# Optimization experiments

Hardware: AMD Instinct MI355X
Metric: run time of the kernel (lower is better)

## Reference

```python
import jax, jax.numpy as jnp
import numpy as np

B, S, HID, NH = 4, 4096, 1024, 16
D = HID // NH
EPS = 1e-5


def setup_inputs() -> dict:
    key = jax.random.key(0)
    ks = jax.random.split(key, 8)
    x = jax.random.normal(ks[0], (B, S, HID), dtype=jnp.float32)
    sc = 0.03  # ~xavier for 1024x1024
    Wq = jax.random.normal(ks[1], (HID, HID), dtype=jnp.float32) * sc
    Wk = jax.random.normal(ks[2], (HID, HID), dtype=jnp.float32) * sc
    Wv = jax.random.normal(ks[3], (HID, HID), dtype=jnp.float32) * sc
    Wbeta = jax.random.normal(ks[4], (HID, NH), dtype=jnp.float32) * sc
    b_beta = jnp.full((NH,), 0.9, dtype=jnp.float32)  # init.constant_(0.9)
    Wo = jax.random.normal(ks[5], (HID, HID), dtype=jnp.float32) * sc
    b_o = jnp.zeros((HID,), dtype=jnp.float32)
    ln_g = jnp.ones((HID,), dtype=jnp.float32)
    ln_b = jnp.zeros((HID,), dtype=jnp.float32)
    return {"x": x, "Wq": Wq, "Wk": Wk, "Wv": Wv, "Wbeta": Wbeta,
            "b_beta": b_beta, "Wo": Wo, "b_o": b_o, "ln_g": ln_g, "ln_b": ln_b}


def _delta_scan(q, k, v, beta):
    # q,k,v: (B,S,NH,D); beta: (B,S,NH)
    # Faithful to torch einsum 'bik,bji->bjk' with broadcast over i:
    # update[b,h,:,k'] = k_t[b,h,k'] * sum_d v_t[b,h,d]  (same row repeated)
    vsum = v.sum(-1)  # (B,S,NH)
    qs = jnp.moveaxis(q, 1, 0)       # (S,B,NH,D)
    ks_ = jnp.moveaxis(k, 1, 0)
    vs = jnp.moveaxis(vsum, 1, 0)    # (S,B,NH)
    bs = jnp.moveaxis(beta, 1, 0)    # (S,B,NH)

    def step(h, inp):
        q_t, k_t, vsum_t, beta_t = inp
        h = h * beta_t[..., None, None]
        h = h + (k_t * vsum_t[..., None])[:, :, None, :]  # broadcast over rows
        o_t = jnp.einsum('bhj,bhjk->bhk', q_t, h)
        return h, o_t

    h0 = jnp.zeros((q.shape[0], q.shape[2], D, D), dtype=q.dtype)
    _, o = jax.lax.scan(step, h0, (qs, ks_, vs, bs))
    return jnp.moveaxis(o, 0, 1)  # (B,S,NH,D)


def reference(x, Wq, Wk, Wv, Wbeta, b_beta, Wo, b_o, ln_g, ln_b):
    b, s, hid = x.shape
    residual = x
    q = (x @ Wq).reshape(b, s, NH, D)
    k = (x @ Wk).reshape(b, s, NH, D)
    v = (x @ Wv).reshape(b, s, NH, D)
    beta = jax.nn.sigmoid(x @ Wbeta + b_beta)  # (B,S,NH)
    o = _delta_scan(q, k, v, beta).reshape(b, s, hid)
    out = o @ Wo + b_o  # dropout is identity in eval
    y = residual + out
    mu = y.mean(-1, keepdims=True)
    var = ((y - mu) ** 2).mean(-1, keepdims=True)
    return ln_g * (y - mu) * jax.lax.rsqrt(var + EPS) + ln_b
```

## Files before the change

### kernel.cpp

```cpp
#include <hip/hip_runtime.h>
#include <hip/hip_bf16.h>

typedef unsigned short u16;
typedef unsigned int   u32;
typedef u32 __attribute__((address_space(1))) gas_u32;
typedef u32 __attribute__((address_space(3))) las_u32;
typedef __bf16 bf16x8 __attribute__((ext_vector_type(8)));
typedef float  f32x4  __attribute__((ext_vector_type(4)));

constexpr int BATCH = 4, SEQ = 4096, HID = 1024, NH = 16, DH = 64;
constexpr int M  = BATCH * SEQ;
constexpr int KD = HID;

__device__ __forceinline__ u16 f2bf(float f) {
  __hip_bfloat16 h = __float2bfloat16(f);
  u16 u; __builtin_memcpy(&u, &h, 2); return u;
}
__device__ __forceinline__ float bf2f(u16 u) {
  u32 x = ((u32)u) << 16; float f; __builtin_memcpy(&f, &x, 4); return f;
}


__global__ __launch_bounds__(256) void transpose_cast(const float* __restrict__ Wk,
                                                      const float* __restrict__ Wo,
                                                      u16* __restrict__ WkT,
                                                      u16* __restrict__ WoT) {
  __shared__ float tile[32][33];
  const float* src = blockIdx.z ? Wo : Wk;
  u16* dst = blockIdx.z ? WoT : WkT;
  int bx = blockIdx.x * 32, by = blockIdx.y * 32;
  int tx = threadIdx.x & 31, ty = threadIdx.x >> 5;
#pragma unroll
  for (int i = 0; i < 4; i++)
    tile[ty + i * 8][tx] = src[(size_t)(by + ty + i * 8) * HID + bx + tx];
  __syncthreads();
#pragma unroll
  for (int i = 0; i < 4; i++)
    dst[(size_t)(bx + ty + i * 8) * HID + by + tx] = f2bf(tile[tx][ty + i * 8]);
}

__global__ __launch_bounds__(256) void build_wsum(const float* __restrict__ Wq,
                                                  const float* __restrict__ Wv,
                                                  const float* __restrict__ Wbeta,
                                                  u16* __restrict__ WsT) {
  int tid = blockIdx.x * 256 + threadIdx.x;
  int c = tid >> 10, kk = tid & 1023;
  float s = 0.f;
  if (c < 16)      { for (int d = 0; d < DH; d++) s += Wq[(size_t)kk * HID + c * DH + d]; }
  else if (c < 32) { for (int d = 0; d < DH; d++) s += Wv[(size_t)kk * HID + (c - 16) * DH + d]; }
  else if (c < 48) { s = Wbeta[(size_t)kk * NH + (c - 32)]; }
  WsT[(size_t)c * HID + kk] = f2bf(s);
}

__global__ __launch_bounds__(256) void skinny_fused(
    const float* __restrict__ x, const u16* __restrict__ Bt,
    const float* __restrict__ bias, float* __restrict__ sq,
    float* __restrict__ sv, float* __restrict__ sb, u16* __restrict__ xb) {
  constexpr int BM = 64, BK = 64;
  __shared__ u16 As[BM * BK];
  __shared__ u16 Bs[64 * BK];
  const int tid = threadIdx.x, wave = tid >> 6, lane = tid & 63;
  const int bm = blockIdx.x;
  const int r16 = lane & 15, hi = lane >> 4;
  const int rsub = lane >> 3, csub = (lane & 7) * 8;
  f32x4 acc[4] = {};
  const float* Ab = x + (size_t)bm * BM * KD;
  u16* xbb = xb + (size_t)bm * BM * KD;

  for (int kt = 0; kt < KD; kt += BK) {
#pragma unroll
    for (int i = 0; i < 2; i++) {
      int slot = wave * 2 + i;
      const u16* g = Bt + (size_t)(slot * 8 + rsub) * KD + kt + csub;
      __builtin_amdgcn_global_load_lds((const gas_u32*)g, (las_u32*)(Bs + slot * 512), 16, 0, 0);
    }
#pragma unroll
    for (int p = 0; p < 2; p++) {
      const int row = p * 32 + (tid >> 3);
      const int c8 = (tid & 7) * 8;
      const float4 u0 = *(const float4*)(Ab + (size_t)row * KD + kt + c8);
      const float4 u1 = *(const float4*)(Ab + (size_t)row * KD + kt + c8 + 4);
      uint4 w;
      w.x = (u32)f2bf(u0.x) | ((u32)f2bf(u0.y) << 16);
      w.y = (u32)f2bf(u0.z) | ((u32)f2bf(u0.w) << 16);
      w.z = (u32)f2bf(u1.x) | ((u32)f2bf(u1.y) << 16);
      w.w = (u32)f2bf(u1.z) | ((u32)f2bf(u1.w) << 16);
      *(uint4*)(As + row * BK + c8) = w;
      *(uint4*)(xbb + (size_t)row * KD + kt + c8) = w;
    }
    __syncthreads();
#pragma unroll
    for (int kk = 0; kk < 2; kk++) {
      bf16x8 af = *(const bf16x8*)(As + (wave * 16 + r16) * BK + kk * 32 + hi * 8);
#pragma unroll
      for (int fn = 0; fn < 4; fn++) {
        bf16x8 bfr = *(const bf16x8*)(Bs + (fn * 16 + r16) * BK + kk * 32 + hi * 8);
        acc[fn] = __builtin_amdgcn_mfma_f32_16x16x32_bf16(af, bfr, acc[fn], 0, 0, 0);
      }
    }
    __syncthreads();
  }

#pragma unroll
  for (int fn = 0; fn < 4; fn++) {
    const int col = fn * 16 + r16;
#pragma unroll
    for (int j = 0; j < 4; j++) {
      const int row = bm * BM + wave * 16 + hi * 4 + j;
      const int b = row >> 12, t = row & 4095;
      float v = acc[fn][j];
      if (col < 16)      sq[((size_t)(b * 16 + col)) * SEQ + t] = v;
      else if (col < 32) sv[((size_t)(b * 16 + col - 16)) * SEQ + t] = v;
      else if (col < 48) {
        float z = v + bias[col - 32];
        sb[((size_t)(b * 16 + col - 32)) * SEQ + t] = 1.f / (1.f + __expf(-z));
      }
    }
  }
}


__device__ __forceinline__ void stage_quarter(const u16* __restrict__ Gk,
                                              int q, u16* lds_tile, int tid, int wave) {
  const int row = q * 64 + (tid >> 3);
  const int s = tid & 7;
  const u16* g = Gk + (size_t)row * KD + (size_t)((s ^ (row & 7)) << 3);
  u16* l = lds_tile + q * 4096 + wave * 512;
  __builtin_amdgcn_global_load_lds((const gas_u32*)g, (las_u32*)l, 16, 0, 0);
}

__device__ __forceinline__ const bf16x8* lds_frag(const u16* lds_tile, int row, int cg) {
  return (const bf16x8*)(lds_tile + ((size_t)row << 6) + (size_t)((cg ^ (row & 7)) << 3));
}

template <int EPI>
__global__ __launch_bounds__(512) void gemm256(
    const u16* __restrict__ A, const u16* __restrict__ Bt, int N,
    u16* __restrict__ Cb, const u16* __restrict__ xres, const float* __restrict__ bias) {
  constexpr int BK = 64, NT = KD / BK;
  __shared__ u16 lds[2][2][16384];
  const int tid = threadIdx.x, wave = tid >> 6, lane = tid & 63;
  const int wm = wave >> 2, wn = wave & 3;
  const int r16 = lane & 15, hi = lane >> 4;
  const int nbn = N >> 8;
  const int bm = (int)blockIdx.x / nbn, bn = (int)blockIdx.x % nbn;
  const u16* Abase = A + (size_t)bm * 256 * KD;
  const u16* Bbase = Bt + (size_t)bn * 256 * KD;

  f32x4 acc[8][4] = {};

  {
    u16* la = &lds[0][0][0]; u16* lb = &lds[0][1][0];
    stage_quarter(Abase, 0, la, tid, wave);
    stage_quarter(Abase, 2, la, tid, wave);
    stage_quarter(Bbase, 0, lb, tid, wave);
    stage_quarter(Bbase, 1, lb, tid, wave);
    stage_quarter(Bbase, 2, lb, tid, wave);
    stage_quarter(Bbase, 3, lb, tid, wave);
    stage_quarter(Abase, 1, la, tid, wave);
    stage_quarter(Abase, 3, la, tid, wave);
  }
  asm volatile("s_waitcnt vmcnt(2)" ::: "memory");
  __builtin_amdgcn_s_barrier();

  for (int kt = 0; kt < NT - 1; ++kt) {
    const int cur = kt & 1;
    const u16* la = &lds[cur][0][0];
    const u16* lb = &lds[cur][1][0];
    u16* na = &lds[cur ^ 1][0][0];
    u16* nb = &lds[cur ^ 1][1][0];
    const u16* An = Abase + (kt + 1) * BK;
    const u16* Bn = Bbase + (kt + 1) * BK;

    bf16x8 bF[4][2];
#pragma unroll
    for (int ph = 0; ph < 4; ++ph) {
      const int mh = ph >> 1;
      const int kk = ph & 1;
      if (ph == 0)      { stage_quarter(An, 0, na, tid, wave); stage_quarter(An, 2, na, tid, wave); }
      else if (ph == 1) { stage_quarter(Bn, 0, nb, tid, wave); stage_quarter(Bn, 1, nb, tid, wave); }
      else if (ph == 2) { stage_quarter(Bn, 2, nb, tid, wave); stage_quarter(Bn, 3, nb, tid, wave); }
      else              { stage_quarter(An, 1, na, tid, wave); stage_quarter(An, 3, na, tid, wave); }
      bf16x8 aF[4];
#pragma unroll
      for (int f = 0; f < 4; ++f)
        aF[f] = *lds_frag(la, wm * 128 + mh * 64 + f * 16 + r16, kk * 4 + hi);
      if (ph < 2) {
#pragma unroll
        for (int g = 0; g < 4; ++g)
          bF[g][kk] = *lds_frag(lb, wn * 64 + g * 16 + r16, kk * 4 + hi);
      }
      __builtin_amdgcn_s_barrier();
      asm volatile("s_waitcnt lgkmcnt(0)" ::: "memory");
      __builtin_amdgcn_sched_barrier(0);
      __builtin_amdgcn_s_setprio(1);
#pragma unroll
      for (int f = 0; f < 4; ++f)
#pragma unroll
        for (int g = 0; g < 4; ++g)
          acc[mh * 4 + f][g] = __builtin_amdgcn_mfma_f32_16x16x32_bf16(
              aF[f], bF[g][kk], acc[mh * 4 + f][g], 0, 0, 0);
      __builtin_amdgcn_s_setprio(0);
      if (ph == 1) { asm volatile("s_waitcnt vmcnt(4)" ::: "memory"); }
      if (ph == 3) { asm volatile("s_waitcnt vmcnt(2)" ::: "memory"); }
      __builtin_amdgcn_s_barrier();
    }
  }

  {
    const u16* la = &lds[(NT - 1) & 1][0][0];
    const u16* lb = &lds[(NT - 1) & 1][1][0];
    bf16x8 bF[4][2];
#pragma unroll
    for (int ph = 0; ph < 4; ++ph) {
      const int mh = ph >> 1, kk = ph & 1;
      bf16x8 aF[4];
#pragma unroll
      for (int f = 0; f < 4; ++f)
        aF[f] = *lds_frag(la, wm * 128 + mh * 64 + f * 16 + r16, kk * 4 + hi);
      if (ph < 2) {
#pragma unroll
        for (int g = 0; g < 4; ++g)
          bF[g][kk] = *lds_frag(lb, wn * 64 + g * 16 + r16, kk * 4 + hi);
      }
      __builtin_amdgcn_s_barrier();
      asm volatile("s_waitcnt lgkmcnt(0)" ::: "memory");
      __builtin_amdgcn_sched_barrier(0);
      __builtin_amdgcn_s_setprio(1);
#pragma unroll
      for (int f = 0; f < 4; ++f)
#pragma unroll
        for (int g = 0; g < 4; ++g)
          acc[mh * 4 + f][g] = __builtin_amdgcn_mfma_f32_16x16x32_bf16(
              aF[f], bF[g][kk], acc[mh * 4 + f][g], 0, 0, 0);
      __builtin_amdgcn_s_setprio(0);
      if (ph == 1) { asm volatile("s_waitcnt vmcnt(0)" ::: "memory"); }
      __builtin_amdgcn_s_barrier();
    }
  }

#pragma unroll
  for (int fm = 0; fm < 8; ++fm) {
#pragma unroll
    for (int fn = 0; fn < 4; ++fn) {
      const int col = bn * 256 + wn * 64 + fn * 16 + r16;
#pragma unroll
      for (int j = 0; j < 4; ++j) {
        const int row = bm * 256 + wm * 128 + fm * 16 + hi * 4 + j;
        float v = acc[fm][fn][j];
        if constexpr (EPI == 2) v += bf2f(xres[(size_t)row * N + col]) + bias[col];
        Cb[(size_t)row * N + col] = f2bf(v);
      }
    }
  }
}


__global__ __launch_bounds__(256) void scan_chunks(const u16* __restrict__ kbuf,
                                                   const float* __restrict__ sv_t,
                                                   const float* __restrict__ sb_t,
                                                   float* __restrict__ Pbuf,
                                                   float* __restrict__ Rloc) {
  const int wave = threadIdx.x >> 6, lane = threadIdx.x & 63;
  const int gid = blockIdx.x * 4 + wave;
  const int seq = gid >> 6, chunk = gid & 63;
  const int b = seq >> 4, h = seq & 15;
  const int t0 = chunk * 64;
  const float bet = sb_t[(size_t)seq * SEQ + t0 + lane];
  const float vs  = sv_t[(size_t)seq * SEQ + t0 + lane];
  const u16* kp = kbuf + ((size_t)(b * SEQ + t0)) * HID + h * DH + lane;
  float r = 0.f, P = 1.f;
#pragma unroll
  for (int tt = 0; tt < 64; tt += 8) {
    u16 kr[8];
#pragma unroll
    for (int j = 0; j < 8; j++) kr[j] = kp[(size_t)(tt + j) * HID];
#pragma unroll
    for (int j = 0; j < 8; j++) {
      float bt = __shfl(bet, tt + j);
      float vt = __shfl(vs, tt + j);
      r = fmaf(r, bt, bf2f(kr[j]) * vt);
      P *= bt;
    }
  }
  Rloc[(size_t)gid * 64 + lane] = r;
  if (lane == 0) Pbuf[gid] = P;
}

__global__ __launch_bounds__(64) void scan_prefix(const float* __restrict__ Pbuf,
                                                  const float* __restrict__ Rloc,
                                                  float* __restrict__ Rin) {
  const int seq = blockIdx.x, lane = threadIdx.x;
  const float* pp = Pbuf + seq * 64;
  const float* rl = Rloc + (size_t)seq * 64 * 64 + lane;
  float* ri = Rin + (size_t)seq * 64 * 64 + lane;
  float rin = 0.f;
#pragma unroll
  for (int c0 = 0; c0 < 64; c0 += 8) {
    float P[8], L[8];
#pragma unroll
    for (int j = 0; j < 8; j++) { P[j] = pp[c0 + j]; L[j] = rl[(size_t)(c0 + j) * 64]; }
#pragma unroll
    for (int j = 0; j < 8; j++) {
      ri[(size_t)(c0 + j) * 64] = rin;
      rin = fmaf(P[j], rin, L[j]);
    }
  }
}

__global__ __launch_bounds__(256) void scan_apply(const u16* __restrict__ kbuf,
                                                  const float* __restrict__ sq_t,
                                                  const float* __restrict__ sv_t,
                                                  const float* __restrict__ sb_t,
                                                  const float* __restrict__ Rin,
                                                  u16* __restrict__ obuf) {
  const int wave = threadIdx.x >> 6, lane = threadIdx.x & 63;
  const int gid = blockIdx.x * 4 + wave;
  const int seq = gid >> 6, chunk = gid & 63;
  const int b = seq >> 4, h = seq & 15;
  const int t0 = chunk * 64;
  const float bet = sb_t[(size_t)seq * SEQ + t0 + lane];
  const float vs  = sv_t[(size_t)seq * SEQ + t0 + lane];
  const float qs  = sq_t[(size_t)seq * SEQ + t0 + lane];
  const u16* kp = kbuf + ((size_t)(b * SEQ + t0)) * HID + h * DH + lane;
  u16* op = obuf + ((size_t)(b * SEQ + t0)) * HID + h * DH + lane;
  float r = Rin[(size_t)gid * 64 + lane];
#pragma unroll
  for (int tt = 0; tt < 64; tt += 8) {
    u16 kr[8];
#pragma unroll
    for (int j = 0; j < 8; j++) kr[j] = kp[(size_t)(tt + j) * HID];
#pragma unroll
    for (int j = 0; j < 8; j++) {
      float bt = __shfl(bet, tt + j);
      float vt = __shfl(vs, tt + j);
      float qt = __shfl(qs, tt + j);
      r = fmaf(r, bt, bf2f(kr[j]) * vt);
      op[(size_t)(tt + j) * HID] = f2bf(qt * r);
    }
  }
}

__global__ __launch_bounds__(256) void ln_kernel(const u16* __restrict__ y,
                                                 const float* __restrict__ g,
                                                 const float* __restrict__ bt,
                                                 float* __restrict__ out) {
  const int row = blockIdx.x;
  const u16* yr = y + (size_t)row * HID;
  const int t = threadIdx.x;
  ushort4 u = *(const ushort4*)(yr + t * 4);
  float v0 = bf2f(u.x), v1 = bf2f(u.y), v2 = bf2f(u.z), v3 = bf2f(u.w);
  float s  = v0 + v1 + v2 + v3;
  float ss = v0 * v0 + v1 * v1 + v2 * v2 + v3 * v3;
#pragma unroll
  for (int m = 1; m < 64; m <<= 1) { s += __shfl_xor(s, m); ss += __shfl_xor(ss, m); }
  __shared__ float red[8];
  const int wave = t >> 6, lane = t & 63;
  if (lane == 0) { red[wave] = s; red[4 + wave] = ss; }
  __syncthreads();
  float st  = red[0] + red[1] + red[2] + red[3];
  float sst = red[4] + red[5] + red[6] + red[7];
  float mu  = st * (1.f / 1024.f);
  float var = sst * (1.f / 1024.f) - mu * mu;
  float inv = rsqrtf(var + 1e-5f);
  const int c = t * 4;
  float4 o;
  o.x = g[c + 0] * ((v0 - mu) * inv) + bt[c + 0];
  o.y = g[c + 1] * ((v1 - mu) * inv) + bt[c + 1];
  o.z = g[c + 2] * ((v2 - mu) * inv) + bt[c + 2];
  o.w = g[c + 3] * ((v3 - mu) * inv) + bt[c + 3];
  *(float4*)(out + (size_t)row * HID + c) = o;
}

extern "C" void kernel_launch(void* const* d_in, const int* in_sizes, int n_in,
                              void* d_out, int out_size, void* d_ws, size_t ws_size,
                              hipStream_t stream) {
  const float* x     = (const float*)d_in[0];
  const float* Wq    = (const float*)d_in[1];
  const float* Wk    = (const float*)d_in[2];
  const float* Wv    = (const float*)d_in[3];
  const float* Wbeta = (const float*)d_in[4];
  const float* bbeta = (const float*)d_in[5];
  const float* Wo    = (const float*)d_in[6];
  const float* b_o   = (const float*)d_in[7];
  const float* ln_g  = (const float*)d_in[8];
  const float* ln_b  = (const float*)d_in[9];
  float* out = (float*)d_out;

  char* ws = (char*)d_ws;
  size_t off = 0;
  auto alloc = [&](size_t bytes) {
    char* p = ws + off; off += (bytes + 255) & ~(size_t)255; return p;
  };
  u16* xb   = (u16*)alloc((size_t)M * HID * 2);
  u16* kbuf = (u16*)alloc((size_t)M * HID * 2);
  u16* obuf = (u16*)alloc((size_t)M * HID * 2);
  u16* WkT  = (u16*)alloc((size_t)HID * HID * 2);
  u16* WoT  = (u16*)alloc((size_t)HID * HID * 2);
  u16* WsT  = (u16*)alloc((size_t)64 * HID * 2);
  float* sq_t = (float*)alloc((size_t)64 * SEQ * 4);
  float* sv_t = (float*)alloc((size_t)64 * SEQ * 4);
  float* sb_t = (float*)alloc((size_t)64 * SEQ * 4);
  float* Pbuf = (float*)alloc((size_t)4096 * 4);
  float* Rloc = (float*)alloc((size_t)4096 * 64 * 4);
  float* Rin  = (float*)alloc((size_t)4096 * 64 * 4);
  u16* ybuf = kbuf;

  transpose_cast<<<dim3(32, 32, 2), 256, 0, stream>>>(Wk, Wo, WkT, WoT);
  build_wsum<<<256, 256, 0, stream>>>(Wq, Wv, Wbeta, WsT);

  skinny_fused<<<M / 64, 256, 0, stream>>>(x, WsT, bbeta, sq_t, sv_t, sb_t, xb);

  gemm256<0><<<(M / 256) * (HID / 256), 512, 0, stream>>>(
      xb, WkT, HID, kbuf, nullptr, nullptr);

  scan_chunks<<<1024, 256, 0, stream>>>(kbuf, sv_t, sb_t, Pbuf, Rloc);
  scan_prefix<<<64, 64, 0, stream>>>(Pbuf, Rloc, Rin);
  scan_apply<<<1024, 256, 0, stream>>>(kbuf, sq_t, sv_t, sb_t, Rin, obuf);

  gemm256<2><<<(M / 256) * (HID / 256), 512, 0, stream>>>(
      obuf, WoT, HID, ybuf, xb, b_o);

  ln_kernel<<<M, 256, 0, stream>>>(ybuf, ln_g, ln_b, out);
}
```

Measured before the change: 158.4 us.

## Merge GEMM main loop phases from four to two per K-tile

Restructures the GEMM inner K-loop from four phases with a barrier each into two half-tile phases. Each phase loads both kk fragments from LDS and issues 32 MFMAs. The explicit lgkmcnt waits and sched_barriers are dropped, so the compiler can interleave LDS reads with MFMAs. This halves the barriers per K-tile and gives longer MFMA runs, at the cost of more live fragment registers, which may hurt occupancy or cause spills.

```diff
diff --git a/kernel.cpp b/kernel.cpp
--- a/kernel.cpp
+++ b/kernel.cpp
@@ -172,71 +172,98 @@
     const u16* An = Abase + (kt + 1) * BK;
     const u16* Bn = Bbase + (kt + 1) * BK;
 
-    bf16x8 bF[4][2];
-#pragma unroll
-    for (int ph = 0; ph < 4; ++ph) {
-      const int mh = ph >> 1;
-      const int kk = ph & 1;
-      if (ph == 0)      { stage_quarter(An, 0, na, tid, wave); stage_quarter(An, 2, na, tid, wave); }
-      else if (ph == 1) { stage_quarter(Bn, 0, nb, tid, wave); stage_quarter(Bn, 1, nb, tid, wave); }
-      else if (ph == 2) { stage_quarter(Bn, 2, nb, tid, wave); stage_quarter(Bn, 3, nb, tid, wave); }
-      else              { stage_quarter(An, 1, na, tid, wave); stage_quarter(An, 3, na, tid, wave); }
-      bf16x8 aF[4];
-#pragma unroll
-      for (int f = 0; f < 4; ++f)
-        aF[f] = *lds_frag(la, wm * 128 + mh * 64 + f * 16 + r16, kk * 4 + hi);
-      if (ph < 2) {
+    stage_quarter(An, 0, na, tid, wave);
+    stage_quarter(An, 2, na, tid, wave);
+    bf16x8 bF[4][2], aF0[4][2];
+#pragma unroll
+    for (int kk = 0; kk < 2; ++kk) {
+#pragma unroll
+      for (int f = 0; f < 4; ++f)
+        aF0[f][kk] = *lds_frag(la, wm * 128 + f * 16 + r16, kk * 4 + hi);
+#pragma unroll
+      for (int g = 0; g < 4; ++g)
+        bF[g][kk] = *lds_frag(lb, wn * 64 + g * 16 + r16, kk * 4 + hi);
+    }
+    stage_quarter(Bn, 0, nb, tid, wave);
+    stage_quarter(Bn, 1, nb, tid, wave);
+    __builtin_amdgcn_s_setprio(1);
+#pragma unroll
+    for (int kk = 0; kk < 2; ++kk)
+#pragma unroll
+      for (int f = 0; f < 4; ++f)
 #pragma unroll
         for (int g = 0; g < 4; ++g)
-          bF[g][kk] = *lds_frag(lb, wn * 64 + g * 16 + r16, kk * 4 + hi);
-      }
-      __builtin_amdgcn_s_barrier();
-      asm volatile("s_waitcnt lgkmcnt(0)" ::: "memory");
-      __builtin_amdgcn_sched_barrier(0);
-      __builtin_amdgcn_s_setprio(1);
+          acc[f][g] = __builtin_amdgcn_mfma_f32_16x16x32_bf16(
+              aF0[f][kk], bF[g][kk], acc[f][g], 0, 0, 0);
+    __builtin_amdgcn_s_setprio(0);
+    asm volatile("s_waitcnt vmcnt(4)" ::: "memory");
+    __builtin_amdgcn_s_barrier();
+
+    stage_quarter(Bn, 2, nb, tid, wave);
+    stage_quarter(Bn, 3, nb, tid, wave);
+    bf16x8 aF1[4][2];
+#pragma unroll
+    for (int kk = 0; kk < 2; ++kk)
+#pragma unroll
+      for (int f = 0; f < 4; ++f)
+        aF1[f][kk] = *lds_frag(la, wm * 128 + 64 + f * 16 + r16, kk * 4 + hi);
+    stage_quarter(An, 1, na, tid, wave);
+    stage_quarter(An, 3, na, tid, wave);
+    __builtin_amdgcn_s_setprio(1);
+#pragma unroll
+    for (int kk = 0; kk < 2; ++kk)
 #pragma unroll
       for (int f = 0; f < 4; ++f)
 #pragma unroll
         for (int g = 0; g < 4; ++g)
-          acc[mh * 4 + f][g] = __builtin_amdgcn_mfma_f32_16x16x32_bf16(
-              aF[f], bF[g][kk], acc[mh * 4 + f][g], 0, 0, 0);
-      __builtin_amdgcn_s_setprio(0);
-      if (ph == 1) { asm volatile("s_waitcnt vmcnt(4)" ::: "memory"); }
-      if (ph == 3) { asm volatile("s_waitcnt vmcnt(2)" ::: "memory"); }
-      __builtin_amdgcn_s_barrier();
-    }
+          acc[4 + f][g] = __builtin_amdgcn_mfma_f32_16x16x32_bf16(
+              aF1[f][kk], bF[g][kk], acc[4 + f][g], 0, 0, 0);
+    __builtin_amdgcn_s_setprio(0);
+    asm volatile("s_waitcnt vmcnt(2)" ::: "memory");
+    __builtin_amdgcn_s_barrier();
   }
 
   {
     const u16* la = &lds[(NT - 1) & 1][0][0];
     const u16* lb = &lds[(NT - 1) & 1][1][0];
-    bf16x8 bF[4][2];
-#pragma unroll
-    for (int ph = 0; ph < 4; ++ph) {
-      const int mh = ph >> 1, kk = ph & 1;
-      bf16x8 aF[4];
-#pragma unroll
-      for (int f = 0; f < 4; ++f)
-        aF[f] = *lds_frag(la, wm * 128 + mh * 64 + f * 16 + r16, kk * 4 + hi);
-      if (ph < 2) {
+    bf16x8 bF[4][2], aF0[4][2];
+#pragma unroll
+    for (int kk = 0; kk < 2; ++kk) {
+#pragma unroll
+      for (int f = 0; f < 4; ++f)
+        aF0[f][kk] = *lds_frag(la, wm * 128 + f * 16 + r16, kk * 4 + hi);
+#pragma unroll
+      for (int g = 0; g < 4; ++g)
+        bF[g][kk] = *lds_frag(lb, wn * 64 + g * 16 + r16, kk * 4 + hi);
+    }
+    __builtin_amdgcn_s_setprio(1);
+#pragma unroll
+    for (int kk = 0; kk < 2; ++kk)
+#pragma unroll
+      for (int f = 0; f < 4; ++f)
 #pragma unroll
         for (int g = 0; g < 4; ++g)
-          bF[g][kk] = *lds_frag(lb, wn * 64 + g * 16 + r16, kk * 4 + hi);
-      }
-      __builtin_amdgcn_s_barrier();
-      asm volatile("s_waitcnt lgkmcnt(0)" ::: "memory");
-      __builtin_amdgcn_sched_barrier(0);
-      __builtin_amdgcn_s_setprio(1);
+          acc[f][g] = __builtin_amdgcn_mfma_f32_16x16x32_bf16(
+              aF0[f][kk], bF[g][kk], acc[f][g], 0, 0, 0);
+    __builtin_amdgcn_s_setprio(0);
+    asm volatile("s_waitcnt vmcnt(0)" ::: "memory");
+    __builtin_amdgcn_s_barrier();
+    bf16x8 aF1[4][2];
+#pragma unroll
+    for (int kk = 0; kk < 2; ++kk)
+#pragma unroll
+      for (int f = 0; f < 4; ++f)
+        aF1[f][kk] = *lds_frag(la, wm * 128 + 64 + f * 16 + r16, kk * 4 + hi);
+    __builtin_amdgcn_s_setprio(1);
+#pragma unroll
+    for (int kk = 0; kk < 2; ++kk)
 #pragma unroll
       for (int f = 0; f < 4; ++f)
 #pragma unroll
         for (int g = 0; g < 4; ++g)
-          acc[mh * 4 + f][g] = __builtin_amdgcn_mfma_f32_16x16x32_bf16(
-              aF[f], bF[g][kk], acc[mh * 4 + f][g], 0, 0, 0);
-      __builtin_amdgcn_s_setprio(0);
-      if (ph == 1) { asm volatile("s_waitcnt vmcnt(0)" ::: "memory"); }
-      __builtin_amdgcn_s_barrier();
-    }
+          acc[4 + f][g] = __builtin_amdgcn_mfma_f32_16x16x32_bf16(
+              aF1[f][kk], bF[g][kk], acc[4 + f][g], 0, 0, 0);
+    __builtin_amdgcn_s_setprio(0);
   }
 
 #pragma unroll
```

Result: slower. 161.7 us (+2.1%).
